# Optimization experiments

Hardware: AMD Instinct MI355X
Metric: run time of the kernel (lower is better)

The kernel has to match this reference:

```python
import jax, jax.numpy as jnp
import numpy as np

K = 20           # top_k
EPS_NORM = 1e-12  # F.normalize default eps


def setup_inputs() -> dict:
    key = jax.random.key(0)
    ks = jax.random.split(key, 16)
    B, C, R, S, SCB, ST, H = 8192, 3755, 214, 13, 30, 6, 64
    return {
        "char_logits": jax.random.normal(ks[0], (B, C), jnp.float32),
        "radical_logits": jax.random.normal(ks[1], (B, R), jnp.float32),
        "structure": jax.random.normal(ks[2], (B, S), jnp.float32),
        "stroke_count": jax.random.normal(ks[3], (B, SCB), jnp.float32),
        "stroke_types": jax.random.normal(ks[4], (B, ST), jnp.float32),
        "radical_mask": jax.random.randint(ks[5], (C, R), 0, 2, jnp.int32),
        "structure_label": jax.random.randint(ks[6], (C,), 0, S, jnp.int32),
        "stroke_count_label": jax.random.randint(ks[7], (C,), 0, SCB, jnp.int32),
        "stroke_type_sig": jax.random.uniform(ks[8], (C, ST), jnp.float32),
        "W1": jax.random.normal(ks[9], (6, H), jnp.float32) * 0.3,
        "b1": jax.random.normal(ks[10], (H,), jnp.float32) * 0.1,
        "W2": jax.random.normal(ks[11], (H, 1), jnp.float32) * 0.3,
        "b2": jax.random.normal(ks[12], (1,), jnp.float32) * 0.1,
        "reranker_weight": jnp.asarray(0.1, jnp.float32),
    }


def _features(char_logits, radical_logits, structure, stroke_count, stroke_types,
              radical_mask, structure_label, stroke_count_label, stroke_type_sig,
              top_idx):
    sg = jax.lax.stop_gradient
    # all model outputs except char_logits are detached by caller; char_logits
    # is detached inside _compute_features for the neural-confidence feature
    rl, st, sc, sty = sg(radical_logits), sg(structure), sg(stroke_count), sg(stroke_types)
    cl_d = sg(char_logits)

    # feature 1/2: radical match & false-alarm ratios
    radical_probs = jax.nn.sigmoid(rl)                              # (B, R)
    cand_mask = radical_mask[top_idx].astype(jnp.float32)           # (B, K, R)
    detected = jnp.einsum('br,bkr->bk', radical_probs, cand_mask)   # (B, K)
    cand_counts = jnp.maximum(cand_mask.sum(-1), 1.0)
    radical_match_ratio = detected / cand_counts
    total_prob = jnp.maximum(radical_probs.sum(-1, keepdims=True), 1e-6)  # (B,1)
    false_alarm_mass = radical_probs.sum(-1, keepdims=True) - detected
    radical_false_ratio = false_alarm_mass / total_prob

    # feature 3: structure match probability
    structure_probs = jax.nn.softmax(st, axis=-1)                   # (B, S)
    cand_structure = structure_label[top_idx]                       # (B, K)
    structure_match = jnp.take_along_axis(structure_probs, cand_structure, axis=1)

    # feature 4: normalized stroke-count distance
    stroke_pred = jnp.argmax(sc, axis=-1)                           # (B,)
    cand_stroke = stroke_count_label[top_idx]                       # (B, K)
    stroke_distance = jnp.abs(stroke_pred[:, None] - cand_stroke).astype(jnp.float32) / 29.0

    # feature 5: zero-masked stroke-type cosine
    cand_sig = stroke_type_sig[top_idx]                             # (B, K, 6)
    sig_norm_val = jnp.linalg.norm(cand_sig, axis=-1)               # (B, K)
    has_sig = (sig_norm_val > 1e-6).astype(jnp.float32)
    pred_norm = sty / jnp.maximum(jnp.linalg.norm(sty, axis=-1, keepdims=True), EPS_NORM)
    cand_adj = cand_sig + 1e-8 * (1.0 - has_sig)[..., None]
    cand_norm = cand_adj / jnp.maximum(jnp.linalg.norm(cand_adj, axis=-1, keepdims=True), EPS_NORM)
    stroke_type_cos = jnp.einsum('bd,bkd->bk', pred_norm, cand_norm) * has_sig

    # feature 6: detached neural confidence
    neural_probs = jax.nn.softmax(cl_d, axis=-1)                    # (B, C)
    neural_conf = jnp.take_along_axis(neural_probs, top_idx, axis=1)

    return jnp.stack([radical_match_ratio, radical_false_ratio, structure_match,
                      stroke_distance, stroke_type_cos, neural_conf], axis=-1)  # (B, K, 6)


def reference(char_logits, radical_logits, structure, stroke_count, stroke_types,
              radical_mask, structure_label, stroke_count_label, stroke_type_sig,
              W1, b1, W2, b2, reranker_weight):
    B = char_logits.shape[0]
    top_logits, top_idx = jax.lax.top_k(char_logits, K)             # (B, K)
    feats = _features(char_logits, radical_logits, structure, stroke_count,
                      stroke_types, radical_mask, structure_label,
                      stroke_count_label, stroke_type_sig, top_idx)
    h = jax.nn.relu(feats @ W1 + b1)                                # (B, K, H)
    rerank_scores = (h @ W2 + b2)[..., 0]                           # (B, K)
    combined_top = top_logits + reranker_weight * rerank_scores
    rows = jnp.arange(B)[:, None]
    return char_logits.at[rows, top_idx].set(combined_top)
```

## Files before the change

kernel.cpp:

```cpp
#include <hip/hip_runtime.h>
#include <math.h>

#define NB   8192
#define NC   3755
#define NR   214
#define NS   13
#define NSC  30
#define NST  6
#define NH   64
#define KTOP 20
#define RPB  4
#define NT   (RPB * 64)
#define NQT  15
#define NBIN 1024
#define CAP  256

__device__ __forceinline__ unsigned sortkey(float x) {
    unsigned u = __float_as_uint(x);
    return (u & 0x80000000u) ? ~u : (u | 0x80000000u);
}

__global__ __launch_bounds__(NT) void reranker_kernel(
    const float* __restrict__ char_logits,
    const float* __restrict__ radical_logits,
    const float* __restrict__ structure,
    const float* __restrict__ stroke_count,
    const float* __restrict__ stroke_types,
    const int*   __restrict__ radical_mask,
    const int*   __restrict__ structure_label,
    const int*   __restrict__ stroke_count_label,
    const float* __restrict__ stroke_type_sig,
    const float* __restrict__ W1,
    const float* __restrict__ b1,
    const float* __restrict__ W2,
    const float* __restrict__ b2,
    const float* __restrict__ rw,
    float*       __restrict__ out)
{
    const int tid  = threadIdx.x;
    const int lane = tid & 63;
    const int wave = tid >> 6;
    const int row  = blockIdx.x * RPB + wave;

    __shared__ unsigned s_hist32[RPB / 2][NBIN];
    __shared__ float s_candv[RPB][CAP];
    __shared__ int   s_candi[RPB][CAP];
    __shared__ float s_probs[RPB][216];
    __shared__ float s_topv[RPB][KTOP];
    __shared__ int   s_topi[RPB][KTOP];
    __shared__ float s_struct[RPB][NS];
    __shared__ float s_aux[RPB][8];
    __shared__ int   s_cnt[RPB];
    __shared__ int   s_need[RPB];

    const int      hw  = wave >> 1;
    const unsigned hsh = (wave & 1) * 16;

    const size_t rowOff = (size_t)row * NC;
    const float* __restrict__ rin  = char_logits + rowOff;
    float*       __restrict__ rout = out + rowOff;

    const int a     = (int)((4 - (rowOff & 3)) & 3);
    const int nq    = (NC - a) >> 2;
    const int ntail = NC - a - 4 * nq;

    int ext_idx = -1;
    if (lane < a)                           ext_idx = lane;
    else if (lane >= 8 && lane < 8 + ntail) ext_idx = a + 4 * nq + (lane - 8);

    float wf[NQT * 4];
#pragma unroll
    for (int t = 0; t < NQT; ++t) {
        int q = lane + t * 64;
        float4 x = make_float4(-INFINITY, -INFINITY, -INFINITY, -INFINITY);
        if (q < nq) {
            x = *reinterpret_cast<const float4*>(rin + a + 4 * q);
            *reinterpret_cast<float4*>(rout + a + 4 * q) = x;
        }
        wf[4*t+0] = x.x; wf[4*t+1] = x.y; wf[4*t+2] = x.z; wf[4*t+3] = x.w;
    }
    float ext = -INFINITY;
    if (ext_idx >= 0) { ext = rin[ext_idx]; rout[ext_idx] = ext; }

    float psum = 0.f;
#pragma unroll
    for (int i = 0; i < 4; ++i) {
        int r = lane + i * 64;
        if (r < NR) {
            float x = radical_logits[(size_t)row * NR + r];
            float pp = 1.f / (1.f + __expf(-x));
            s_probs[wave][r] = pp;
            psum += pp;
        }
    }

    if (lane == 0) {
        float sv[NS]; float m = -INFINITY;
#pragma unroll
        for (int i = 0; i < NS; ++i) { sv[i] = structure[(size_t)row * NS + i]; m = fmaxf(m, sv[i]); }
        float s = 0.f;
#pragma unroll
        for (int i = 0; i < NS; ++i) { sv[i] = __expf(sv[i] - m); s += sv[i]; }
        float inv = 1.f / s;
#pragma unroll
        for (int i = 0; i < NS; ++i) s_struct[wave][i] = sv[i] * inv;
    } else if (lane == 1) {
        float bv = -INFINITY; int bi = 0;
#pragma unroll
        for (int i = 0; i < NSC; ++i) {
            float x = stroke_count[(size_t)row * NSC + i];
            if (x > bv) { bv = x; bi = i; }
        }
        s_aux[wave][6] = (float)bi;
    } else if (lane == 2) {
        float t6[NST]; float ss = 0.f;
#pragma unroll
        for (int i = 0; i < NST; ++i) { t6[i] = stroke_types[(size_t)row * NST + i]; ss += t6[i] * t6[i]; }
        float inv = 1.f / fmaxf(sqrtf(ss), 1e-12f);
#pragma unroll
        for (int i = 0; i < NST; ++i) s_aux[wave][i] = t6[i] * inv;
    } else if (lane == 3) {
        s_cnt[wave] = 0;
    }

    float m0 = ext, m1 = -INFINITY, m2 = -INFINITY, m3 = -INFINITY;
#pragma unroll
    for (int t = 0; t < NQT; ++t) {
        m0 = fmaxf(m0, wf[4*t+0]); m1 = fmaxf(m1, wf[4*t+1]);
        m2 = fmaxf(m2, wf[4*t+2]); m3 = fmaxf(m3, wf[4*t+3]);
    }
    float lmax = fmaxf(fmaxf(m0, m1), fmaxf(m2, m3));
#pragma unroll
    for (int off = 32; off > 0; off >>= 1) lmax = fmaxf(lmax, __shfl_xor(lmax, off));
    const float rowmax = lmax;

    for (int i = tid; i < (RPB / 2) * NBIN; i += NT)
        (&s_hist32[0][0])[i] = 0u;
    __syncthreads();

    const unsigned floork1 = 0xBF800000u;
#pragma unroll
    for (int t = 0; t < NQT; ++t) {
        int q = lane + t * 64;
        if (q < nq) {
#pragma unroll
            for (int j = 0; j < 4; ++j) {
                unsigned k = sortkey(wf[4*t+j]);
                if (k >= floork1) atomicAdd(&s_hist32[hw][k >> 22], 1u << hsh);
            }
        }
    }
    if (ext_idx >= 0) {
        unsigned k = sortkey(ext);
        if (k >= floork1) atomicAdd(&s_hist32[hw][k >> 22], 1u << hsh);
    }
    __syncthreads();

    int B0 = -1;
    {
        int bb = (int)(sortkey(rowmax) >> 22);
        int fb = (int)(floork1 >> 22);
        int cum = 0;
        while (bb >= fb) {
            cum += (int)((s_hist32[hw][bb] >> hsh) & 0xFFFFu);
            if (cum >= KTOP) break;
            --bb;
        }
        B0 = (cum >= KTOP) ? bb : -1;
    }
    const int need2 = (B0 < 0) ? 1 : 0;
    if (lane == 0) s_need[wave] = need2;
    __syncthreads();

    const int any2 = s_need[0] | s_need[1] | s_need[2] | s_need[3];
    if (any2) {
        if (need2) {
#pragma unroll
            for (int i = 0; i < NBIN / 64; ++i) s_hist32[hw][lane + i * 64] = 0u;
        }
        __syncthreads();
        if (need2) {
#pragma unroll
            for (int t = 0; t < NQT; ++t) {
                int q = lane + t * 64;
                if (q < nq) {
#pragma unroll
                    for (int j = 0; j < 4; ++j) {
                        unsigned k = sortkey(wf[4*t+j]);
                        atomicAdd(&s_hist32[hw][k >> 22], 1u << hsh);
                    }
                }
            }
            if (ext_idx >= 0) atomicAdd(&s_hist32[hw][sortkey(ext) >> 22], 1u << hsh);
        }
        __syncthreads();
        if (need2) {
            int bb = (int)(sortkey(rowmax) >> 22);
            int cum = 0;
            while (bb >= 0) {
                cum += (int)((s_hist32[hw][bb] >> hsh) & 0xFFFFu);
                if (cum >= KTOP) break;
                --bb;
            }
            B0 = bb;
        }
    }

#pragma unroll
    for (int t = 0; t < NQT; ++t) {
        int q = lane + t * 64;
        if (q < nq) {
#pragma unroll
            for (int j = 0; j < 4; ++j) {
                float x = wf[4*t+j];
                if ((int)(sortkey(x) >> 22) >= B0) {
                    int pos = atomicAdd(&s_cnt[wave], 1);
                    if (pos < CAP) { s_candv[wave][pos] = x; s_candi[wave][pos] = a + 4*q + j; }
                }
            }
        }
    }
    if (ext_idx >= 0 && (int)(sortkey(ext) >> 22) >= B0) {
        int pos = atomicAdd(&s_cnt[wave], 1);
        if (pos < CAP) { s_candv[wave][pos] = ext; s_candi[wave][pos] = ext_idx; }
    }
    __syncthreads();
    int M = s_cnt[wave]; if (M > CAP) M = CAP;

    for (int c = lane; c < M; c += 64) {
        float cv = s_candv[wave][c]; int ci = s_candi[wave][c];
        int rank = 0;
        for (int j = 0; j < M; ++j) {
            float ov = s_candv[wave][j]; int oi = s_candi[wave][j];
            rank += (ov > cv || (ov == cv && oi < ci)) ? 1 : 0;
        }
        if (rank < KTOP) { s_topv[wave][rank] = cv; s_topi[wave][rank] = ci; }
    }
    __syncthreads();

    float e0 = __expf(ext - rowmax), e1 = 0.f, e2 = 0.f, e3 = 0.f;
#pragma unroll
    for (int t = 0; t < NQT; ++t) {
        e0 += __expf(wf[4*t+0] - rowmax);
        e1 += __expf(wf[4*t+1] - rowmax);
        e2 += __expf(wf[4*t+2] - rowmax);
        e3 += __expf(wf[4*t+3] - rowmax);
    }
    float le = (e0 + e1) + (e2 + e3);
#pragma unroll
    for (int off = 32; off > 0; off >>= 1) le += __shfl_xor(le, off);
    const float sumexp = le;
#pragma unroll
    for (int off = 32; off > 0; off >>= 1) psum += __shfl_xor(psum, off);
    const float total = psum;

    const float b1v = b1[lane];
    float w1v[6];
#pragma unroll
    for (int j = 0; j < 6; ++j) w1v[j] = W1[j * NH + lane];
    const float w2v = W2[lane];
    const float b2v = b2[0];
    const float wrk = rw[0];
    const float spred = s_aux[wave][6];
    float predv[NST];
#pragma unroll
    for (int i = 0; i < NST; ++i) predv[i] = s_aux[wave][i];


    for (int k = 0; k < KTOP; ++k) {
        const int   ci = __builtin_amdgcn_readfirstlane(s_topi[wave][k]);
        const float tv = s_topv[wave][k];
        const int* __restrict__ mrow = radical_mask + (size_t)ci * NR;
        float det = 0.f, cnt = 0.f;
#pragma unroll
        for (int i = 0; i < 4; ++i) {
            int r = lane + i * 64;
            if (r < NR) {
                float m = (float)mrow[r];
                det += s_probs[wave][r] * m;
                cnt += m;
            }
        }
#pragma unroll
        for (int off = 32; off > 0; off >>= 1) {
            det += __shfl_xor(det, off);
            cnt += __shfl_xor(cnt, off);
        }
        float f1 = det / fmaxf(cnt, 1.f);
        float f2 = (total - det) / fmaxf(total, 1e-6f);
        float f3 = s_struct[wave][structure_label[ci]];
        float f4 = fabsf(spred - (float)stroke_count_label[ci]) * (1.f / 29.f);
        float sig[NST]; float ss = 0.f;
#pragma unroll
        for (int i = 0; i < NST; ++i) { sig[i] = stroke_type_sig[(size_t)ci * NST + i]; ss += sig[i] * sig[i]; }
        float nrm = sqrtf(ss);
        float has = (nrm > 1e-6f) ? 1.f : 0.f;
        float add = 1e-8f * (1.f - has);
        float ss2 = 0.f;
#pragma unroll
        for (int i = 0; i < NST; ++i) { sig[i] += add; ss2 += sig[i] * sig[i]; }
        float inv = 1.f / fmaxf(sqrtf(ss2), 1e-12f);
        float dot = 0.f;
#pragma unroll
        for (int i = 0; i < NST; ++i) dot += predv[i] * sig[i] * inv;
        float f5 = dot * has;
        float f6 = __expf(tv - rowmax) / sumexp;

        float acc = b1v + f1 * w1v[0] + f2 * w1v[1] + f3 * w1v[2]
                        + f4 * w1v[3] + f5 * w1v[4] + f6 * w1v[5];
        float h = fmaxf(acc, 0.f);
        float part = h * w2v;
#pragma unroll
        for (int off = 32; off > 0; off >>= 1) part += __shfl_xor(part, off);
        if (lane == 0) rout[ci] = tv + wrk * (part + b2v);
    }
}

extern "C" void kernel_launch(void* const* d_in, const int* in_sizes, int n_in,
                              void* d_out, int out_size, void* d_ws, size_t ws_size,
                              hipStream_t stream) {
    (void)in_sizes; (void)n_in; (void)out_size; (void)d_ws; (void)ws_size;
    const float* char_logits        = (const float*)d_in[0];
    const float* radical_logits     = (const float*)d_in[1];
    const float* structure          = (const float*)d_in[2];
    const float* stroke_count       = (const float*)d_in[3];
    const float* stroke_types       = (const float*)d_in[4];
    const int*   radical_mask       = (const int*)d_in[5];
    const int*   structure_label    = (const int*)d_in[6];
    const int*   stroke_count_label = (const int*)d_in[7];
    const float* stroke_type_sig    = (const float*)d_in[8];
    const float* W1                 = (const float*)d_in[9];
    const float* b1                 = (const float*)d_in[10];
    const float* W2                 = (const float*)d_in[11];
    const float* b2                 = (const float*)d_in[12];
    const float* rw                 = (const float*)d_in[13];
    float* out = (float*)d_out;

    reranker_kernel<<<NB / RPB, NT, 0, stream>>>(
        char_logits, radical_logits, structure, stroke_count, stroke_types,
        radical_mask, structure_label, stroke_count_label, stroke_type_sig,
        W1, b1, W2, b2, rw, out);
}
```

Measured before the change: 404.6 us.

## Stream row logits from global memory instead of caching them in registers

Drops the 60-float per-lane register cache of each char_logits row. The histogram pass now loads, copies and bins each float4 while also taking the max, and later passes reload the row from global/L2 for candidate selection (fused with the softmax sum) and for the fallback histogram. Launch bounds now request 8 blocks per unit and CAP shrinks to 192, both aimed at lower register and LDS pressure and higher occupancy. The cost is re-reading each row two or three times and a smaller candidate buffer.

New measurement: 405.7 us. Within noise of the previous version (+0.3%).

```diff
diff --git a/kernel.cpp b/kernel.cpp
--- a/kernel.cpp
+++ b/kernel.cpp
@@ -13,14 +13,14 @@
 #define NT   (RPB * 64)
 #define NQT  15
 #define NBIN 1024
-#define CAP  256
+#define CAP  192
 
 __device__ __forceinline__ unsigned sortkey(float x) {
     unsigned u = __float_as_uint(x);
     return (u & 0x80000000u) ? ~u : (u | 0x80000000u);
 }
 
-__global__ __launch_bounds__(NT) void reranker_kernel(
+__global__ __launch_bounds__(NT, 8) void reranker_kernel(
     const float* __restrict__ char_logits,
     const float* __restrict__ radical_logits,
     const float* __restrict__ structure,
@@ -68,19 +68,9 @@
     if (lane < a)                           ext_idx = lane;
     else if (lane >= 8 && lane < 8 + ntail) ext_idx = a + 4 * nq + (lane - 8);
 
-    float wf[NQT * 4];
-#pragma unroll
-    for (int t = 0; t < NQT; ++t) {
-        int q = lane + t * 64;
-        float4 x = make_float4(-INFINITY, -INFINITY, -INFINITY, -INFINITY);
-        if (q < nq) {
-            x = *reinterpret_cast<const float4*>(rin + a + 4 * q);
-            *reinterpret_cast<float4*>(rout + a + 4 * q) = x;
-        }
-        wf[4*t+0] = x.x; wf[4*t+1] = x.y; wf[4*t+2] = x.z; wf[4*t+3] = x.w;
-    }
-    float ext = -INFINITY;
-    if (ext_idx >= 0) { ext = rin[ext_idx]; rout[ext_idx] = ext; }
+    for (int i = tid; i < (RPB / 2) * NBIN; i += NT)
+        (&s_hist32[0][0])[i] = 0u;
+    if (tid < RPB) s_cnt[tid] = 0;
 
     float psum = 0.f;
 #pragma unroll
@@ -119,41 +109,36 @@
         float inv = 1.f / fmaxf(sqrtf(ss), 1e-12f);
 #pragma unroll
         for (int i = 0; i < NST; ++i) s_aux[wave][i] = t6[i] * inv;
-    } else if (lane == 3) {
-        s_cnt[wave] = 0;
-    }
-
-    float m0 = ext, m1 = -INFINITY, m2 = -INFINITY, m3 = -INFINITY;
-#pragma unroll
-    for (int t = 0; t < NQT; ++t) {
-        m0 = fmaxf(m0, wf[4*t+0]); m1 = fmaxf(m1, wf[4*t+1]);
-        m2 = fmaxf(m2, wf[4*t+2]); m3 = fmaxf(m3, wf[4*t+3]);
-    }
-    float lmax = fmaxf(fmaxf(m0, m1), fmaxf(m2, m3));
-#pragma unroll
-    for (int off = 32; off > 0; off >>= 1) lmax = fmaxf(lmax, __shfl_xor(lmax, off));
-    const float rowmax = lmax;
-
-    for (int i = tid; i < (RPB / 2) * NBIN; i += NT)
-        (&s_hist32[0][0])[i] = 0u;
+    }
     __syncthreads();
 
     const unsigned floork1 = 0xBF800000u;
-#pragma unroll
+    float m0 = -INFINITY, m1 = -INFINITY, m2 = -INFINITY, m3 = -INFINITY;
+    float ext = -INFINITY;
+    if (ext_idx >= 0) {
+        ext = rin[ext_idx]; rout[ext_idx] = ext;
+        unsigned k = sortkey(ext);
+        if (k >= floork1) atomicAdd(&s_hist32[hw][k >> 22], 1u << hsh);
+    }
     for (int t = 0; t < NQT; ++t) {
         int q = lane + t * 64;
         if (q < nq) {
-#pragma unroll
-            for (int j = 0; j < 4; ++j) {
-                unsigned k = sortkey(wf[4*t+j]);
-                if (k >= floork1) atomicAdd(&s_hist32[hw][k >> 22], 1u << hsh);
-            }
-        }
-    }
-    if (ext_idx >= 0) {
-        unsigned k = sortkey(ext);
-        if (k >= floork1) atomicAdd(&s_hist32[hw][k >> 22], 1u << hsh);
-    }
+            float4 x = *reinterpret_cast<const float4*>(rin + a + 4 * q);
+            *reinterpret_cast<float4*>(rout + a + 4 * q) = x;
+            m0 = fmaxf(m0, x.x); m1 = fmaxf(m1, x.y);
+            m2 = fmaxf(m2, x.z); m3 = fmaxf(m3, x.w);
+            unsigned k0 = sortkey(x.x), k1 = sortkey(x.y);
+            unsigned k2 = sortkey(x.z), k3 = sortkey(x.w);
+            if (k0 >= floork1) atomicAdd(&s_hist32[hw][k0 >> 22], 1u << hsh);
+            if (k1 >= floork1) atomicAdd(&s_hist32[hw][k1 >> 22], 1u << hsh);
+            if (k2 >= floork1) atomicAdd(&s_hist32[hw][k2 >> 22], 1u << hsh);
+            if (k3 >= floork1) atomicAdd(&s_hist32[hw][k3 >> 22], 1u << hsh);
+        }
+    }
+    float lmax = fmaxf(fmaxf(m0, m1), fmaxf(fmaxf(m2, m3), ext));
+#pragma unroll
+    for (int off = 32; off > 0; off >>= 1) lmax = fmaxf(lmax, __shfl_xor(lmax, off));
+    const float rowmax = lmax;
     __syncthreads();
 
     int B0 = -1;
@@ -180,15 +165,14 @@
         }
         __syncthreads();
         if (need2) {
-#pragma unroll
             for (int t = 0; t < NQT; ++t) {
                 int q = lane + t * 64;
                 if (q < nq) {
-#pragma unroll
-                    for (int j = 0; j < 4; ++j) {
-                        unsigned k = sortkey(wf[4*t+j]);
-                        atomicAdd(&s_hist32[hw][k >> 22], 1u << hsh);
-                    }
+                    float4 x = *reinterpret_cast<const float4*>(rin + a + 4 * q);
+                    atomicAdd(&s_hist32[hw][sortkey(x.x) >> 22], 1u << hsh);
+                    atomicAdd(&s_hist32[hw][sortkey(x.y) >> 22], 1u << hsh);
+                    atomicAdd(&s_hist32[hw][sortkey(x.z) >> 22], 1u << hsh);
+                    atomicAdd(&s_hist32[hw][sortkey(x.w) >> 22], 1u << hsh);
                 }
             }
             if (ext_idx >= 0) atomicAdd(&s_hist32[hw][sortkey(ext) >> 22], 1u << hsh);
@@ -206,25 +190,49 @@
         }
     }
 
-#pragma unroll
+    float e0 = 0.f, e1 = 0.f, e2 = 0.f, e3 = 0.f;
+    if (ext_idx >= 0) {
+        e0 = __expf(ext - rowmax);
+        if ((int)(sortkey(ext) >> 22) >= B0) {
+            int pos = atomicAdd(&s_cnt[wave], 1);
+            if (pos < CAP) { s_candv[wave][pos] = ext; s_candi[wave][pos] = ext_idx; }
+        }
+    }
     for (int t = 0; t < NQT; ++t) {
         int q = lane + t * 64;
         if (q < nq) {
-#pragma unroll
-            for (int j = 0; j < 4; ++j) {
-                float x = wf[4*t+j];
-                if ((int)(sortkey(x) >> 22) >= B0) {
-                    int pos = atomicAdd(&s_cnt[wave], 1);
-                    if (pos < CAP) { s_candv[wave][pos] = x; s_candi[wave][pos] = a + 4*q + j; }
-                }
-            }
-        }
-    }
-    if (ext_idx >= 0 && (int)(sortkey(ext) >> 22) >= B0) {
-        int pos = atomicAdd(&s_cnt[wave], 1);
-        if (pos < CAP) { s_candv[wave][pos] = ext; s_candi[wave][pos] = ext_idx; }
-    }
-    __syncthreads();
+            float4 x = *reinterpret_cast<const float4*>(rin + a + 4 * q);
+            e0 += __expf(x.x - rowmax);
+            e1 += __expf(x.y - rowmax);
+            e2 += __expf(x.z - rowmax);
+            e3 += __expf(x.w - rowmax);
+            if ((int)(sortkey(x.x) >> 22) >= B0) {
+                int pos = atomicAdd(&s_cnt[wave], 1);
+                if (pos < CAP) { s_candv[wave][pos] = x.x; s_candi[wave][pos] = a + 4*q + 0; }
+            }
+            if ((int)(sortkey(x.y) >> 22) >= B0) {
+                int pos = atomicAdd(&s_cnt[wave], 1);
+                if (pos < CAP) { s_candv[wave][pos] = x.y; s_candi[wave][pos] = a + 4*q + 1; }
+            }
+            if ((int)(sortkey(x.z) >> 22) >= B0) {
+                int pos = atomicAdd(&s_cnt[wave], 1);
+                if (pos < CAP) { s_candv[wave][pos] = x.z; s_candi[wave][pos] = a + 4*q + 2; }
+            }
+            if ((int)(sortkey(x.w) >> 22) >= B0) {
+                int pos = atomicAdd(&s_cnt[wave], 1);
+                if (pos < CAP) { s_candv[wave][pos] = x.w; s_candi[wave][pos] = a + 4*q + 3; }
+            }
+        }
+    }
+    float le = (e0 + e1) + (e2 + e3);
+#pragma unroll
+    for (int off = 32; off > 0; off >>= 1) le += __shfl_xor(le, off);
+    const float sumexp = le;
+#pragma unroll
+    for (int off = 32; off > 0; off >>= 1) psum += __shfl_xor(psum, off);
+    const float total = psum;
+    __syncthreads();
+
     int M = s_cnt[wave]; if (M > CAP) M = CAP;
 
     for (int c = lane; c < M; c += 64) {
@@ -238,22 +246,6 @@
     }
     __syncthreads();
 
-    float e0 = __expf(ext - rowmax), e1 = 0.f, e2 = 0.f, e3 = 0.f;
-#pragma unroll
-    for (int t = 0; t < NQT; ++t) {
-        e0 += __expf(wf[4*t+0] - rowmax);
-        e1 += __expf(wf[4*t+1] - rowmax);
-        e2 += __expf(wf[4*t+2] - rowmax);
-        e3 += __expf(wf[4*t+3] - rowmax);
-    }
-    float le = (e0 + e1) + (e2 + e3);
-#pragma unroll
-    for (int off = 32; off > 0; off >>= 1) le += __shfl_xor(le, off);
-    const float sumexp = le;
-#pragma unroll
-    for (int off = 32; off > 0; off >>= 1) psum += __shfl_xor(psum, off);
-    const float total = psum;
-
     const float b1v = b1[lane];
     float w1v[6];
 #pragma unroll
@@ -262,10 +254,6 @@
     const float b2v = b2[0];
     const float wrk = rw[0];
     const float spred = s_aux[wave][6];
-    float predv[NST];
-#pragma unroll
-    for (int i = 0; i < NST; ++i) predv[i] = s_aux[wave][i];
-
 
     for (int k = 0; k < KTOP; ++k) {
         const int   ci = __builtin_amdgcn_readfirstlane(s_topi[wave][k]);
@@ -302,7 +290,7 @@
         float inv = 1.f / fmaxf(sqrtf(ss2), 1e-12f);
         float dot = 0.f;
 #pragma unroll
-        for (int i = 0; i < NST; ++i) dot += predv[i] * sig[i] * inv;
+        for (int i = 0; i < NST; ++i) dot += s_aux[wave][i] * sig[i] * inv;
         float f5 = dot * has;
         float f6 = __expf(tv - rowmax) / sumexp;
 
@@ -323,7 +311,7 @@
     const float* char_logits        = (const float*)d_in[0];
     const float* radical_logits     = (const float*)d_in[1];
     const float* structure          = (const float*)d_in[2];
-    const float* stroke_count       = (const float*)d_in[3];
+    const float* stroke_count      = (const float*)d_in[3];
     const float* stroke_types       = (const float*)d_in[4];
     const int*   radical_mask       = (const int*)d_in[5];
     const int*   structure_label    = (const int*)d_in[6];
```
